# Optimization experiments

Measured on AMD Instinct MI355X. Metric: run time of the kernel, lower is better.

## Reference

```python
import jax, jax.numpy as jnp
import numpy as np
import math

# Config constants (from init_kwargs)
KV_CHANNELS = 128
NUM_HEADS = 32
NUM_KV_HEADS = 2
LAYER_NUMBER = 2  # apply_query_key_layer_scaling=True -> coeff = layer_number
HEAD_DIM = KV_CHANNELS
HIDDEN = KV_CHANNELS * NUM_HEADS
COEFF = float(LAYER_NUMBER)
NORM_FACTOR = math.sqrt(HEAD_DIM) * COEFF


def setup_inputs() -> dict:
    key = jax.random.key(0)
    k1, k2, k3, k4 = jax.random.split(key, 4)
    B, Q, KV = 2, 2048, 2048
    query_layer = jax.random.normal(k1, (B, NUM_HEADS, Q, HEAD_DIM), dtype=jnp.float32)
    key_layer = jax.random.normal(k2, (B, NUM_KV_HEADS, KV, HEAD_DIM), dtype=jnp.float32)
    value_layer = jax.random.normal(k3, (B, NUM_KV_HEADS, KV, HEAD_DIM), dtype=jnp.float32)
    attention_mask = jax.random.normal(k4, (B, 1, Q, KV), dtype=jnp.float32)
    return {
        "query_layer": query_layer,
        "key_layer": key_layer,
        "value_layer": value_layer,
        "attention_mask": attention_mask,
    }


def reference(query_layer, key_layer, value_layer, attention_mask):
    # Fallback (non-FusedSDPA) path of CoreAttention.forward, eval mode (no dropout).
    b, h, q_len, d = query_layer.shape
    g = key_layer.shape[1]          # num_key_value_heads
    r = h // g                      # n_rep
    # gaudi_chatglm_repeat_kv: grouped view (b, g, r, q, d) vs kv (b, g, kv, d)
    qg = query_layer.reshape(b, g, r, q_len, d)
    # scores: (b, g, r, q, kv)
    scores = jnp.einsum("bgrqd,bgkd->bgrqk", qg, key_layer) / NORM_FACTOR
    scores = scores * COEFF
    # mask unsqueezed at dim 1 -> (b, 1, 1, q, kv), broadcast-add
    scores = scores + attention_mask[:, None]
    # softmax in fp32, cast back to query dtype
    attn = jax.nn.softmax(scores.astype(jnp.float32), axis=-1).astype(query_layer.dtype)
    # AV: (b, g, r, q, d)
    out = jnp.einsum("bgrqk,bgkd->bgrqd", attn, value_layer)
    out = out.reshape(b, h, q_len, d)
    # permute (2,0,1,3) -> (q, b, h, d); reshape -> (q, b, hidden)
    context = jnp.transpose(out, (2, 0, 1, 3)).reshape(q_len, b, h * d)
    return context
```

## Files before the change

### kernel.cpp

```cpp
#include <hip/hip_runtime.h>
#include <hip/hip_bf16.h>


constexpr int Bn = 2, Hn = 32, Gn = 2, Qn = 2048, KVn = 2048, Dn = 128;
constexpr int WAVES = 8, QBLK = 32, HO = 8;
constexpr int KVB = 64, NT = KVn / KVB;
constexpr int NT32 = KVn / 32;
constexpr float SCALE = 0.08838834764831843f;
constexpr float L2E = 1.4426950408889634f;
constexpr float SCALE2 = SCALE * L2E;

constexpr size_t WSK_BYTES = (size_t)Bn * Gn * KVn * 256;

typedef __attribute__((ext_vector_type(16))) float f32x16;
typedef __attribute__((ext_vector_type(8))) __bf16 bf16x8;
typedef __attribute__((ext_vector_type(2))) unsigned u32x2;

__device__ __forceinline__ unsigned pk2(float a, float b) {
  union { __bf16 h[2]; unsigned u; } x;
  x.h[0] = (__bf16)a; x.h[1] = (__bf16)b;
  return x.u;
}

__global__ __launch_bounds__(256)
void prepack(const float* __restrict__ Kg, const float* __restrict__ Vg,
             char* __restrict__ wsK, char* __restrict__ wsV) {
  const int i = blockIdx.x * 256 + threadIdx.x;
  {
    const int dp = i & 63, kv = (i >> 6) & (KVn - 1), bg = i >> 17;
    const float* src = Kg + ((size_t)bg * KVn + kv) * Dn + 2 * dp;
    const unsigned pr = pk2(src[0], src[1]);
    const size_t off = (size_t)bg * (KVn * 256) + (size_t)kv * 256
                       + ((4 * dp) ^ ((kv & 15) << 4));
    *(unsigned*)(wsK + off) = pr;
  }
  {
    const int d = i & 127, vg = (i >> 7) & 1023, bg = i >> 17;
    const int t = vg >> 4, vkp = vg & 15;
    const float* src = Vg + ((size_t)bg * KVn + t * 32 + 2 * vkp) * Dn + d;
    const unsigned pr = pk2(src[0], src[Dn]);
    const int slot = (((d >> 3) ^ (d >> 1)) & 3) << 4;
    const size_t off = ((size_t)bg * NT32 + t) * 8192 + (d << 6)
                       + ((vkp * 4) ^ slot);
    *(unsigned*)(wsV + off) = pr;
  }
}

__global__ __launch_bounds__(512, 2)
void attn_fwd(const float* __restrict__ Qg, const float* __restrict__ Mg,
              const char* __restrict__ wsK, const char* __restrict__ wsV,
              float* __restrict__ Og) {
  __shared__ __align__(16) short Ks[2][KVB * Dn];
  __shared__ __align__(16) short Vt[2][Dn * KVB];
  __shared__ __align__(16) float Ms[2][QBLK * KVB];

  const int tid = threadIdx.x;
  const int lane = tid & 63, w = tid >> 6;
  const int hi = lane >> 5, ln = lane & 31;
  const int qb = blockIdx.x * QBLK, ho = blockIdx.y, b = blockIdx.z;
  const int h = ho * HO + w;
  const int g = ho >> 1, bg = b * Gn + g;

  bf16x8 aq[8];
  {
    const float* qr = Qg + ((size_t)(b * Hn + h) * Qn + qb + ln) * Dn + hi * 8;
#pragma unroll
    for (int ks = 0; ks < 8; ++ks) {
      float4 f0 = *(const float4*)(qr + ks * 16);
      float4 f1 = *(const float4*)(qr + ks * 16 + 4);
      union { unsigned u[4]; bf16x8 b; } t;
      t.u[0] = pk2(f0.x * SCALE2, f0.y * SCALE2);
      t.u[1] = pk2(f0.z * SCALE2, f0.w * SCALE2);
      t.u[2] = pk2(f1.x * SCALE2, f1.y * SCALE2);
      t.u[3] = pk2(f1.z * SCALE2, f1.w * SCALE2);
      aq[ks] = t.b;
    }
  }

  const char* wsKb = wsK + (size_t)bg * (KVn * 256);
  const char* wsVb = wsV + (size_t)bg * (KVn * 256);
  const int mr = w * 4 + (lane >> 4);
  const int mc = (lane & 15) << 4;
  const char* pM0 = (const char*)Mg + (size_t)(b * Qn + qb + mr) * (KVn * 4)
                    + (mc ^ ((mr & 15) << 4));
  const char* pK = wsKb + w * 2048 + lane * 16;
  const char* pV = wsVb + w * 2048 + lane * 16;
  const char* pM = pM0;
  char* dK0 = (char*)Ks[0] + w * 2048; char* dK1 = (char*)Ks[1] + w * 2048;
  char* dV0 = (char*)Vt[0] + w * 2048; char* dV1 = (char*)Vt[1] + w * 2048;
  char* dM0 = (char*)Ms[0] + w * 1024; char* dM1 = (char*)Ms[1] + w * 1024;

  auto gll = [](const char* s, char* d) {
    __builtin_amdgcn_global_load_lds(
        (const __attribute__((address_space(1))) void*)s,
        (__attribute__((address_space(3))) void*)d, 16, 0, 0);
  };
  auto stageK = [&](char* dk) { gll(pK, dk); gll(pK + 1024, dk + 1024); };
  auto stageVM = [&](char* dv, char* dm) {
    gll(pV, dv); gll(pV + 1024, dv + 1024); gll(pM, dm);
  };

  const int ksw = (ln & 15) << 4;
  const int msw = (ln & 15) << 4;
  const char* msb0 = (const char*)Ms[0] + ln * 256;
  const char* msb1 = (const char*)Ms[1] + ln * 256;

  auto qk = [&](const char* ksb, f32x16& t0, f32x16& t1) {
#pragma unroll
    for (int e = 0; e < 16; ++e) { t0[e] = 0.0f; t1[e] = 0.0f; }
    __builtin_amdgcn_s_setprio(1);
#pragma unroll
    for (int ks = 0; ks < 8; ++ks) {
      const int byte = (ks * 32 + hi * 16) ^ ksw;
      bf16x8 k0 = *(const bf16x8*)(ksb + (ln << 8) + byte);
      bf16x8 k1 = *(const bf16x8*)(ksb + ((32 + ln) << 8) + byte);
      t0 = __builtin_amdgcn_mfma_f32_32x32x16_bf16(k0, aq[ks], t0, 0, 0, 0);
      t1 = __builtin_amdgcn_mfma_f32_32x32x16_bf16(k1, aq[ks], t1, 0, 0, 0);
    }
    __builtin_amdgcn_s_setprio(0);
  };

  f32x16 o[4];
#pragma unroll
  for (int nt = 0; nt < 4; ++nt)
#pragma unroll
    for (int e = 0; e < 16; ++e) o[nt][e] = 0.0f;
  float lsum = 0.0f;

  auto body = [&](int t, f32x16& sC0, f32x16& sC1, f32x16& sN0, f32x16& sN1) {
    const int cur = t & 1;

    stageK(cur ? dK1 : dK0);
    stageVM(cur ? dV0 : dV1, cur ? dM0 : dM1);
    if (t + 3 < NT) pK += 16384;
    if (t + 2 < NT) { pV += 16384; pM += 256; }
    __builtin_amdgcn_sched_barrier(0);

    const char* msb = cur ? msb1 : msb0;
    unsigned own0[8], own1[8];
    float psum = 0.0f;
#pragma unroll
    for (int gq = 0; gq < 4; ++gq) {
      float4 m0 = *(const float4*)(msb + ((gq * 32 + hi * 16) ^ msw));
      float4 m1 = *(const float4*)(msb + ((128 + gq * 32 + hi * 16) ^ msw));
      float p0 = __builtin_exp2f(__builtin_fmaf(m0.x, L2E, sC0[4 * gq + 0]));
      float p1 = __builtin_exp2f(__builtin_fmaf(m0.y, L2E, sC0[4 * gq + 1]));
      float p2 = __builtin_exp2f(__builtin_fmaf(m0.z, L2E, sC0[4 * gq + 2]));
      float p3 = __builtin_exp2f(__builtin_fmaf(m0.w, L2E, sC0[4 * gq + 3]));
      float q0 = __builtin_exp2f(__builtin_fmaf(m1.x, L2E, sC1[4 * gq + 0]));
      float q1 = __builtin_exp2f(__builtin_fmaf(m1.y, L2E, sC1[4 * gq + 1]));
      float q2 = __builtin_exp2f(__builtin_fmaf(m1.z, L2E, sC1[4 * gq + 2]));
      float q3 = __builtin_exp2f(__builtin_fmaf(m1.w, L2E, sC1[4 * gq + 3]));
      psum += ((p0 + p1) + (p2 + p3)) + ((q0 + q1) + (q2 + q3));
      own0[2 * gq] = pk2(p0, p1); own0[2 * gq + 1] = pk2(p2, p3);
      own1[2 * gq] = pk2(q0, q1); own1[2 * gq + 1] = pk2(q2, q3);
    }
    lsum += psum;

    qk((const char*)Ks[cur ^ 1], sN0, sN1);

    union Frag { unsigned u[4]; bf16x8 b; };
    Frag pf[4];
#pragma unroll
    for (int ks = 0; ks < 4; ++ks) {
      const unsigned* ow = (ks < 2) ? own0 : own1;
      const int bsl = (ks & 1) * 4;
#if __has_builtin(__builtin_amdgcn_permlane32_swap)
      u32x2 r0 = __builtin_amdgcn_permlane32_swap(ow[bsl + 0], ow[bsl + 2], false, false);
      u32x2 r1 = __builtin_amdgcn_permlane32_swap(ow[bsl + 1], ow[bsl + 3], false, false);
      pf[ks].u[0] = r0.x; pf[ks].u[2] = r0.y;
      pf[ks].u[1] = r1.x; pf[ks].u[3] = r1.y;
#else
      unsigned sA = __shfl_xor(ow[bsl + 0], 32), sCx = __shfl_xor(ow[bsl + 2], 32);
      unsigned sB = __shfl_xor(ow[bsl + 1], 32), sD = __shfl_xor(ow[bsl + 3], 32);
      pf[ks].u[0] = hi ? sCx : ow[bsl + 0];
      pf[ks].u[1] = hi ? sD : ow[bsl + 1];
      pf[ks].u[2] = hi ? ow[bsl + 2] : sA;
      pf[ks].u[3] = hi ? ow[bsl + 3] : sB;
#endif
    }

    const char* vtb = (const char*)Vt[cur];
    __builtin_amdgcn_s_setprio(1);
#pragma unroll
    for (int nt = 0; nt < 4; ++nt) {
      const int d = nt * 32 + ln;
      const int swz = (((d >> 3) ^ (d >> 1)) & 3) << 4;
#pragma unroll
      for (int ks = 0; ks < 4; ++ks) {
        const int base = (ks >> 1) * 8192 + (d << 6);
        bf16x8 vfr = *(const bf16x8*)(vtb + base + (((ks & 1) * 32 + hi * 16) ^ swz));
        o[nt] = __builtin_amdgcn_mfma_f32_32x32x16_bf16(vfr, pf[ks].b, o[nt], 0, 0, 0);
      }
    }
    __builtin_amdgcn_s_setprio(0);

    __syncthreads();
  };

  stageK(dK0); pK += 16384;
  stageK(dK1); pK += 16384;
  stageVM(dV0, dM0); pV += 16384; pM += 256;
  __syncthreads();
  f32x16 sA0, sA1, sB0, sB1;
  qk((const char*)Ks[0], sA0, sA1);
  __syncthreads();

  for (int t = 0; t < NT; t += 2) {
    body(t, sA0, sA1, sB0, sB1);
    body(t + 1, sB0, sB1, sA0, sA1);
  }

  const float ltot = lsum + __shfl_xor(lsum, 32);
  const float invl = 1.0f / ltot;
  float* outp = Og + (size_t)(qb + ln) * (Bn * Hn * Dn) + (size_t)b * (Hn * Dn) + h * Dn;
#pragma unroll
  for (int nt = 0; nt < 4; ++nt)
#pragma unroll
    for (int gq = 0; gq < 4; ++gq) {
      float4 v;
      v.x = o[nt][gq * 4 + 0] * invl;
      v.y = o[nt][gq * 4 + 1] * invl;
      v.z = o[nt][gq * 4 + 2] * invl;
      v.w = o[nt][gq * 4 + 3] * invl;
      *(float4*)(outp + nt * 32 + gq * 8 + hi * 4) = v;
    }
}

extern "C" void kernel_launch(void* const* d_in, const int* in_sizes, int n_in,
                              void* d_out, int out_size, void* d_ws, size_t ws_size,
                              hipStream_t stream) {
  const float* q = (const float*)d_in[0];
  const float* k = (const float*)d_in[1];
  const float* v = (const float*)d_in[2];
  const float* m = (const float*)d_in[3];
  float* out = (float*)d_out;
  char* wsK = (char*)d_ws;
  char* wsV = wsK + WSK_BYTES;

  prepack<<<dim3((Bn * Gn * KVn * 64) / 256), 256, 0, stream>>>(k, v, wsK, wsV);
  dim3 grid(Qn / QBLK, Hn / HO, Bn);
  attn_fwd<<<grid, WAVES * 64, 0, stream>>>(q, m, wsK, wsV, out);
}
```

Baseline: 217.5 us.

## Defer PV matmul by one tile to overlap softmax with MFMA

Restructures the pipeline so the P·V MFMA for tile t-1 is issued right after the QK MFMA for tile t+1, while the P fragments for tile t are built afterward and carried to the next iteration. V staging moves to a 4-deep LDS ring to keep the older V tile resident, with a zeroed slot and zeroed initial P fragments making the first deferred PV a no-op, plus an epilogue for the final tile. The setprio hints around the MFMA loops are removed. LDS use doubles for V, which may reduce occupancy, and register pressure grows because two sets of P fragments are live.

New measurement: 228.9 us. 1.05x slower.

```diff
diff --git a/kernel.cpp b/kernel.cpp
--- a/kernel.cpp
+++ b/kernel.cpp
@@ -15,6 +15,8 @@
 typedef __attribute__((ext_vector_type(16))) float f32x16;
 typedef __attribute__((ext_vector_type(8))) __bf16 bf16x8;
 typedef __attribute__((ext_vector_type(2))) unsigned u32x2;
+
+union Frag { unsigned u[4]; bf16x8 b; };
 
 __device__ __forceinline__ unsigned pk2(float a, float b) {
   union { __bf16 h[2]; unsigned u; } x;
@@ -51,7 +53,7 @@
               const char* __restrict__ wsK, const char* __restrict__ wsV,
               float* __restrict__ Og) {
   __shared__ __align__(16) short Ks[2][KVB * Dn];
-  __shared__ __align__(16) short Vt[2][Dn * KVB];
+  __shared__ __align__(16) short Vt[4][Dn * KVB];
   __shared__ __align__(16) float Ms[2][QBLK * KVB];
 
   const int tid = threadIdx.x;
@@ -81,13 +83,13 @@
   const char* wsVb = wsV + (size_t)bg * (KVn * 256);
   const int mr = w * 4 + (lane >> 4);
   const int mc = (lane & 15) << 4;
-  const char* pM0 = (const char*)Mg + (size_t)(b * Qn + qb + mr) * (KVn * 4)
-                    + (mc ^ ((mr & 15) << 4));
   const char* pK = wsKb + w * 2048 + lane * 16;
   const char* pV = wsVb + w * 2048 + lane * 16;
-  const char* pM = pM0;
+  const char* pM = (const char*)Mg + (size_t)(b * Qn + qb + mr) * (KVn * 4)
+                   + (mc ^ ((mr & 15) << 4));
   char* dK0 = (char*)Ks[0] + w * 2048; char* dK1 = (char*)Ks[1] + w * 2048;
-  char* dV0 = (char*)Vt[0] + w * 2048; char* dV1 = (char*)Vt[1] + w * 2048;
+  char* const vtBase = (char*)Vt[0];
+  char* const dVw = vtBase + w * 2048;
   char* dM0 = (char*)Ms[0] + w * 1024; char* dM1 = (char*)Ms[1] + w * 1024;
 
   auto gll = [](const char* s, char* d) {
@@ -96,9 +98,6 @@
         (__attribute__((address_space(3))) void*)d, 16, 0, 0);
   };
   auto stageK = [&](char* dk) { gll(pK, dk); gll(pK + 1024, dk + 1024); };
-  auto stageVM = [&](char* dv, char* dm) {
-    gll(pV, dv); gll(pV + 1024, dv + 1024); gll(pM, dm);
-  };
 
   const int ksw = (ln & 15) << 4;
   const int msw = (ln & 15) << 4;
@@ -108,7 +107,6 @@
   auto qk = [&](const char* ksb, f32x16& t0, f32x16& t1) {
 #pragma unroll
     for (int e = 0; e < 16; ++e) { t0[e] = 0.0f; t1[e] = 0.0f; }
-    __builtin_amdgcn_s_setprio(1);
 #pragma unroll
     for (int ks = 0; ks < 8; ++ks) {
       const int byte = (ks * 32 + hi * 16) ^ ksw;
@@ -117,7 +115,6 @@
       t0 = __builtin_amdgcn_mfma_f32_32x32x16_bf16(k0, aq[ks], t0, 0, 0, 0);
       t1 = __builtin_amdgcn_mfma_f32_32x32x16_bf16(k1, aq[ks], t1, 0, 0, 0);
     }
-    __builtin_amdgcn_s_setprio(0);
   };
 
   f32x16 o[4];
@@ -127,11 +124,16 @@
     for (int e = 0; e < 16; ++e) o[nt][e] = 0.0f;
   float lsum = 0.0f;
 
-  auto body = [&](int t, f32x16& sC0, f32x16& sC1, f32x16& sN0, f32x16& sN1) {
+  auto body = [&](int t, f32x16& sC0, f32x16& sC1, f32x16& sN0, f32x16& sN1,
+                  Frag (&pfPrev)[4], Frag (&pfCur)[4]) {
     const int cur = t & 1;
 
     stageK(cur ? dK1 : dK0);
-    stageVM(cur ? dV0 : dV1, cur ? dM0 : dM1);
+    {
+      char* dv = dVw + ((t + 1) & 3) * 16384;
+      gll(pV, dv); gll(pV + 1024, dv + 1024);
+      gll(pM, cur ? dM0 : dM1);
+    }
     if (t + 3 < NT) pK += 16384;
     if (t + 2 < NT) { pV += 16384; pM += 256; }
     __builtin_amdgcn_sched_barrier(0);
@@ -159,8 +161,21 @@
 
     qk((const char*)Ks[cur ^ 1], sN0, sN1);
 
-    union Frag { unsigned u[4]; bf16x8 b; };
-    Frag pf[4];
+    {
+      const char* vtb = vtBase + ((t + 3) & 3) * 16384;
+#pragma unroll
+      for (int nt = 0; nt < 4; ++nt) {
+        const int d = nt * 32 + ln;
+        const int swz = (((d >> 3) ^ (d >> 1)) & 3) << 4;
+#pragma unroll
+        for (int ks = 0; ks < 4; ++ks) {
+          const int base = (ks >> 1) * 8192 + (d << 6);
+          bf16x8 vfr = *(const bf16x8*)(vtb + base + (((ks & 1) * 32 + hi * 16) ^ swz));
+          o[nt] = __builtin_amdgcn_mfma_f32_32x32x16_bf16(vfr, pfPrev[ks].b, o[nt], 0, 0, 0);
+        }
+      }
+    }
+
 #pragma unroll
     for (int ks = 0; ks < 4; ++ks) {
       const unsigned* ow = (ks < 2) ? own0 : own1;
@@ -168,47 +183,62 @@
 #if __has_builtin(__builtin_amdgcn_permlane32_swap)
       u32x2 r0 = __builtin_amdgcn_permlane32_swap(ow[bsl + 0], ow[bsl + 2], false, false);
       u32x2 r1 = __builtin_amdgcn_permlane32_swap(ow[bsl + 1], ow[bsl + 3], false, false);
-      pf[ks].u[0] = r0.x; pf[ks].u[2] = r0.y;
-      pf[ks].u[1] = r1.x; pf[ks].u[3] = r1.y;
+      pfCur[ks].u[0] = r0.x; pfCur[ks].u[2] = r0.y;
+      pfCur[ks].u[1] = r1.x; pfCur[ks].u[3] = r1.y;
 #else
       unsigned sA = __shfl_xor(ow[bsl + 0], 32), sCx = __shfl_xor(ow[bsl + 2], 32);
       unsigned sB = __shfl_xor(ow[bsl + 1], 32), sD = __shfl_xor(ow[bsl + 3], 32);
-      pf[ks].u[0] = hi ? sCx : ow[bsl + 0];
-      pf[ks].u[1] = hi ? sD : ow[bsl + 1];
-      pf[ks].u[2] = hi ? ow[bsl + 2] : sA;
-      pf[ks].u[3] = hi ? ow[bsl + 3] : sB;
+      pfCur[ks].u[0] = hi ? sCx : ow[bsl + 0];
+      pfCur[ks].u[1] = hi ? sD : ow[bsl + 1];
+      pfCur[ks].u[2] = hi ? ow[bsl + 2] : sA;
+      pfCur[ks].u[3] = hi ? ow[bsl + 3] : sB;
 #endif
     }
-
-    const char* vtb = (const char*)Vt[cur];
-    __builtin_amdgcn_s_setprio(1);
-#pragma unroll
-    for (int nt = 0; nt < 4; ++nt) {
-      const int d = nt * 32 + ln;
-      const int swz = (((d >> 3) ^ (d >> 1)) & 3) << 4;
-#pragma unroll
-      for (int ks = 0; ks < 4; ++ks) {
-        const int base = (ks >> 1) * 8192 + (d << 6);
-        bf16x8 vfr = *(const bf16x8*)(vtb + base + (((ks & 1) * 32 + hi * 16) ^ swz));
-        o[nt] = __builtin_amdgcn_mfma_f32_32x32x16_bf16(vfr, pf[ks].b, o[nt], 0, 0, 0);
-      }
-    }
-    __builtin_amdgcn_s_setprio(0);
 
     __syncthreads();
   };
 
   stageK(dK0); pK += 16384;
   stageK(dK1); pK += 16384;
-  stageVM(dV0, dM0); pV += 16384; pM += 256;
+  {
+    gll(pV, dVw); gll(pV + 1024, dVw + 1024);
+    gll(pM, dM0);
+    pV += 16384; pM += 256;
+  }
+  {
+    char* z = vtBase + 3 * 16384 + tid * 32;
+    *(uint4*)z = make_uint4(0, 0, 0, 0);
+    *(uint4*)(z + 16) = make_uint4(0, 0, 0, 0);
+  }
   __syncthreads();
   f32x16 sA0, sA1, sB0, sB1;
   qk((const char*)Ks[0], sA0, sA1);
   __syncthreads();
 
+  Frag pfA[4], pfB[4];
+#pragma unroll
+  for (int i = 0; i < 4; ++i) {
+    pfA[i].u[0] = 0; pfA[i].u[1] = 0; pfA[i].u[2] = 0; pfA[i].u[3] = 0;
+  }
+
   for (int t = 0; t < NT; t += 2) {
-    body(t, sA0, sA1, sB0, sB1);
-    body(t + 1, sB0, sB1, sA0, sA1);
+    body(t,     sA0, sA1, sB0, sB1, pfA, pfB);
+    body(t + 1, sB0, sB1, sA0, sA1, pfB, pfA);
+  }
+
+  {
+    const char* vtb = vtBase + ((NT - 1) & 3) * 16384;
+#pragma unroll
+    for (int nt = 0; nt < 4; ++nt) {
+      const int d = nt * 32 + ln;
+      const int swz = (((d >> 3) ^ (d >> 1)) & 3) << 4;
+#pragma unroll
+      for (int ks = 0; ks < 4; ++ks) {
+        const int base = (ks >> 1) * 8192 + (d << 6);
+        bf16x8 vfr = *(const bf16x8*)(vtb + base + (((ks & 1) * 32 + hi * 16) ^ swz));
+        o[nt] = __builtin_amdgcn_mfma_f32_32x32x16_bf16(vfr, pfA[ks].b, o[nt], 0, 0, 0);
+      }
+    }
   }
 
   const float ltot = lsum + __shfl_xor(lsum, 32);
```
